# Optimization experiments

Hardware: AMD Instinct MI355X
Metric: run time of the kernel (lower is better)

The kernel has to match this reference:

```python
import jax, jax.numpy as jnp
import numpy as np

B, D, O = 8192, 64, 256

def setup_inputs() -> dict:
    key = jax.random.key(0)
    k1, k2, k3 = jax.random.split(key, 3)
    x = jax.random.normal(k1, (B, D), dtype=jnp.float32)
    centers = jax.random.uniform(k2, (O, 1, D), dtype=jnp.float32)  # RandomUniform(0,1)
    # Original uses Constant(10.0) which saturates exp(-quad) to 0; use small random
    # betas so the quadratic form is in a numerically meaningful range.
    betas = jax.random.normal(k3, (O, D, D), dtype=jnp.float32) * 0.05
    return {"x": x, "centers": centers, "betas": betas}

def reference(x, centers, betas):
    # precision[o] = betas[o] @ betas[o]^T   -> [O, D, D]
    precision = jnp.einsum('ode,ofe->odf', betas, betas)
    # diff[o,b,:] = centers[o] - x[b]        -> [O, B, D]
    diff = centers - x[None, :, :]
    # quad[o,b] = diff[o,b]^T P[o] diff[o,b] -> [O, B]
    quad = jnp.einsum('obd,odf,obf->ob', diff, precision, diff)
    return jnp.exp(-quad).T  # [B, O]
```

## Files before the change

kernel.cpp:

```cpp
#include <hip/hip_runtime.h>
#include <hip/hip_bf16.h>

typedef __bf16 bf16x8 __attribute__((ext_vector_type(8)));
typedef float  f32x4  __attribute__((ext_vector_type(4)));
typedef float  f32x16 __attribute__((ext_vector_type(16)));

constexpr int Bn = 8192, Dn = 64, On = 256;

#define GLD16(g, l) __builtin_amdgcn_global_load_lds( \
    (const __attribute__((address_space(1))) void*)(g), \
    (__attribute__((address_space(3))) void*)(l), 16, 0, 0)

__global__ void k_prep(const float* __restrict__ betas, const float* __restrict__ centers,
                       __bf16* __restrict__ bTsw, float* __restrict__ ncpk) {
    __shared__ float s[64 * 65];
    const int o = blockIdx.x, tid = threadIdx.x;
    const float* bo = betas + (size_t)o * 4096;
    for (int j = tid; j < 1024; j += 256) {
        int d = j >> 4, e4 = (j & 15) * 4;
        float4 v = ((const float4*)bo)[j];
        s[d * 65 + e4 + 0] = v.x; s[d * 65 + e4 + 1] = v.y;
        s[d * 65 + e4 + 2] = v.z; s[d * 65 + e4 + 3] = v.w;
    }
    __syncthreads();
    for (int p = tid; p < 4096; p += 256) {
        int chunk = p >> 3, j = p & 7;
        int ek = chunk >> 6, lane = chunk & 63;
        int e = (ek >> 2) * 32 + (lane & 31);
        int d = ((ek & 3) * 2 + (lane >> 5)) * 8 + j;
        bTsw[(size_t)o * 4096 + p] = (__bf16)s[d * 65 + e];
    }
    if (tid < 64) {
        int et = tid >> 5, rem = tid & 31, l5 = rem >> 4, reg = rem & 15;
        int row = et * 32 + l5 * 4 + (reg & 3) + ((reg >> 2) << 3);
        float acc = 0.f;
        for (int d = 0; d < 64; ++d) acc += s[d * 65 + row] * centers[o * 64 + d];
        ncpk[o * 64 + tid] = -acc;
    }
}

__global__ void __launch_bounds__(256, 4)
k_main(const float* __restrict__ x, const __bf16* __restrict__ bTsw,
       const float* __restrict__ ncpk, float* __restrict__ out) {
    __shared__ __align__(16) unsigned char smem[2 * 8192 + 2048];
    __bf16* sA0 = (__bf16*)smem;
    __bf16* sA1 = (__bf16*)(smem + 8192);
    float*  sCp = (float*)(smem + 16384);

    const int tid = threadIdx.x, wq = tid >> 6, lane = tid & 63;
    const int l31 = lane & 31, l5 = lane >> 5;
    const int bbase = blockIdx.x * 256;
    const int o0 = blockIdx.y * 8;

    sCp[tid]       = ncpk[o0 * 64 + tid];
    sCp[256 + tid] = ncpk[o0 * 64 + 256 + tid];

    bf16x8 xf[2][4];
#pragma unroll
    for (int bt = 0; bt < 2; ++bt)
#pragma unroll
        for (int kk = 0; kk < 4; ++kk) {
            const float* xp = x + (size_t)(bbase + wq * 64 + bt * 32 + l31) * 64
                                + (kk * 2 + l5) * 8;
            float4 v0 = *(const float4*)xp, v1 = *(const float4*)(xp + 4);
            bf16x8 f;
            f[0] = (__bf16)v0.x; f[1] = (__bf16)v0.y; f[2] = (__bf16)v0.z; f[3] = (__bf16)v0.w;
            f[4] = (__bf16)v1.x; f[5] = (__bf16)v1.y; f[6] = (__bf16)v1.z; f[7] = (__bf16)v1.w;
            xf[bt][kk] = f;
        }

    auto prefetch = [&](int o, __bf16* buf) {
        const __bf16* g = bTsw + (size_t)o * 4096;
        GLD16(g + (size_t)(wq * 128 + lane) * 8,      buf + (wq * 128) * 8);
        GLD16(g + (size_t)(wq * 128 + 64 + lane) * 8, buf + (wq * 128 + 64) * 8);
    };

    float qd[8];
    prefetch(o0, sA0);
    __builtin_amdgcn_s_waitcnt(0x0f70);
    __syncthreads();

#pragma unroll
    for (int oi = 0; oi < 8; ++oi) {
        __bf16* cur = (oi & 1) ? sA1 : sA0;
        if (oi < 7) prefetch(o0 + oi + 1, (oi & 1) ? sA0 : sA1);

        f32x4 qv[2] = {{0,0,0,0},{0,0,0,0}};
#pragma unroll
        for (int et = 0; et < 2; ++et) {
            f32x16 cpv;
#pragma unroll
            for (int r4 = 0; r4 < 4; ++r4)
                ((f32x4*)&cpv)[r4] = *(const f32x4*)(sCp + oi * 64 + et * 32 + l5 * 16 + r4 * 4);
            bf16x8 af[4];
#pragma unroll
            for (int k = 0; k < 4; ++k)
                af[k] = *(const bf16x8*)(cur + (size_t)((et * 4 + k) * 64 + lane) * 8);
#pragma unroll
            for (int bt = 0; bt < 2; ++bt) {
                f32x16 acc = __builtin_amdgcn_mfma_f32_32x32x16_bf16(af[0], xf[bt][0], cpv, 0, 0, 0);
                acc = __builtin_amdgcn_mfma_f32_32x32x16_bf16(af[1], xf[bt][1], acc, 0, 0, 0);
                acc = __builtin_amdgcn_mfma_f32_32x32x16_bf16(af[2], xf[bt][2], acc, 0, 0, 0);
                acc = __builtin_amdgcn_mfma_f32_32x32x16_bf16(af[3], xf[bt][3], acc, 0, 0, 0);
                const f32x4* aq = (const f32x4*)&acc;
                qv[bt] += aq[0] * aq[0];
                qv[bt] += aq[1] * aq[1];
                qv[bt] += aq[2] * aq[2];
                qv[bt] += aq[3] * aq[3];
            }
        }
        float q0 = (qv[0][0] + qv[0][1]) + (qv[0][2] + qv[0][3]);
        float q1 = (qv[1][0] + qv[1][1]) + (qv[1][2] + qv[1][3]);
        q0 += __shfl_xor(q0, 32, 64);
        q1 += __shfl_xor(q1, 32, 64);
        qd[oi] = l5 ? q1 : q0;

        __builtin_amdgcn_sched_barrier(0);
        __builtin_amdgcn_s_waitcnt(0x0f70);
        __syncthreads();
    }
    __syncthreads();

    float* scr = (float*)smem;
    {
        int r = wq * 64 + l5 * 32 + l31;
#pragma unroll
        for (int oi = 0; oi < 8; ++oi) scr[r * 12 + oi] = qd[oi];
    }
    __syncthreads();
    {
        const float* q8 = scr + tid * 12;
        f32x4 r0 = *(const f32x4*)q8, r1 = *(const f32x4*)(q8 + 4);
        f32x4 e0, e1;
#pragma unroll
        for (int j = 0; j < 4; ++j) { e0[j] = __expf(-r0[j]); e1[j] = __expf(-r1[j]); }
        float* op = out + (size_t)(bbase + tid) * 256 + o0;
        *(f32x4*)op       = e0;
        *(f32x4*)(op + 4) = e1;
    }
}

extern "C" void kernel_launch(void* const* d_in, const int* in_sizes, int n_in,
                              void* d_out, int out_size, void* d_ws, size_t ws_size,
                              hipStream_t stream) {
    const float* x       = (const float*)d_in[0];
    const float* centers = (const float*)d_in[1];
    const float* betas   = (const float*)d_in[2];
    float* out = (float*)d_out;

    char* ws = (char*)d_ws;
    __bf16* bTsw = (__bf16*)ws;
    float*  ncpk = (float*)(ws + 2 * (1 << 20));

    k_prep<<<dim3(On),                dim3(256), 0, stream>>>(betas, centers, bTsw, ncpk);
    k_main<<<dim3(Bn / 256, On / 8),  dim3(256), 0, stream>>>(x, bTsw, ncpk, out);
}
```

Measured before the change: 89.00 us.

## Expand quadratic form to drop per-output center loads and LDS epilogue

Rewrites the quadratic form as ||B^T x||^2 - 2 x·(B B^T c) + ||B^T c||^2. The main loop's MFMA accumulators therefore start from zero instead of per-output center projections loaded from LDS every iteration. The linear term is computed once per block with a few extra MFMAs, using hi/lo bf16-split weights prepared in k_prep. The constant term is precomputed in fp32. The redundant LDS round-trip in the epilogue is removed, and the affine term is combined via a lane shuffle. The risk is numerical cancellation from the expanded form, with x still quantized to bf16.

```diff
diff --git a/kernel.cpp b/kernel.cpp
--- a/kernel.cpp
+++ b/kernel.cpp
@@ -11,9 +11,15 @@
     (const __attribute__((address_space(1))) void*)(g), \
     (__attribute__((address_space(3))) void*)(l), 16, 0, 0)
 
+__device__ __forceinline__ int apos(int m, int d) {
+    return (((d >> 4) * 64) + (((d >> 3) & 1) * 32) + m) * 8 + (d & 7);
+}
+
 __global__ void k_prep(const float* __restrict__ betas, const float* __restrict__ centers,
-                       __bf16* __restrict__ bTsw, float* __restrict__ ncpk) {
+                       __bf16* __restrict__ bTsw, __bf16* __restrict__ waffT,
+                       float* __restrict__ kt) {
     __shared__ float s[64 * 65];
+    __shared__ float cp[64];
     const int o = blockIdx.x, tid = threadIdx.x;
     const float* bo = betas + (size_t)o * 4096;
     for (int j = tid; j < 1024; j += 256) {
@@ -21,6 +27,12 @@
         float4 v = ((const float4*)bo)[j];
         s[d * 65 + e4 + 0] = v.x; s[d * 65 + e4 + 1] = v.y;
         s[d * 65 + e4 + 2] = v.z; s[d * 65 + e4 + 3] = v.w;
+    }
+    __syncthreads();
+    if (tid < 64) {
+        float a = 0.f;
+        for (int d = 0; d < 64; ++d) a += s[d * 65 + tid] * centers[o * 64 + d];
+        cp[tid] = a;
     }
     __syncthreads();
     for (int p = tid; p < 4096; p += 256) {
@@ -31,29 +43,41 @@
         bTsw[(size_t)o * 4096 + p] = (__bf16)s[d * 65 + e];
     }
     if (tid < 64) {
-        int et = tid >> 5, rem = tid & 31, l5 = rem >> 4, reg = rem & 15;
-        int row = et * 32 + l5 * 4 + (reg & 3) + ((reg >> 2) << 3);
-        float acc = 0.f;
-        for (int d = 0; d < 64; ++d) acc += s[d * 65 + row] * centers[o * 64 + d];
-        ncpk[o * 64 + tid] = -acc;
+        int d = tid;
+        float w = 0.f;
+        for (int e = 0; e < 64; ++e) w += s[d * 65 + e] * cp[e];
+        w *= -2.f;
+        __bf16 hi = (__bf16)w;
+        __bf16 lo = (__bf16)(w - (float)hi);
+        size_t base = (size_t)(o >> 3) * 2048;
+        int m = o & 7;
+        waffT[base + apos(m, d)]      = hi;
+        waffT[base + apos(8 + m, d)]  = lo;
+        int mz = 16 + 2 * m;
+        waffT[base + apos(mz, d)]     = (__bf16)0.f;
+        waffT[base + apos(mz + 1, d)] = (__bf16)0.f;
+    }
+    if (tid == 0) {
+        float s2 = 0.f;
+        for (int e = 0; e < 64; ++e) s2 += cp[e] * cp[e];
+        kt[o] = s2;
     }
 }
 
 __global__ void __launch_bounds__(256, 4)
 k_main(const float* __restrict__ x, const __bf16* __restrict__ bTsw,
-       const float* __restrict__ ncpk, float* __restrict__ out) {
-    __shared__ __align__(16) unsigned char smem[2 * 8192 + 2048];
-    __bf16* sA0 = (__bf16*)smem;
-    __bf16* sA1 = (__bf16*)(smem + 8192);
-    float*  sCp = (float*)(smem + 16384);
+       const __bf16* __restrict__ waffT, const float* __restrict__ kt,
+       float* __restrict__ out) {
+    __shared__ __align__(16) __bf16 sA[2 * 4096];
+    __shared__ float sZero[4];
 
     const int tid = threadIdx.x, wq = tid >> 6, lane = tid & 63;
     const int l31 = lane & 31, l5 = lane >> 5;
     const int bbase = blockIdx.x * 256;
-    const int o0 = blockIdx.y * 8;
+    const int og = blockIdx.y;
+    const int o0 = og * 8;
 
-    sCp[tid]       = ncpk[o0 * 64 + tid];
-    sCp[256 + tid] = ncpk[o0 * 64 + 256 + tid];
+    if (tid < 4) sZero[tid] = 0.f;
 
     bf16x8 xf[2][4];
 #pragma unroll
@@ -68,6 +92,10 @@
             f[4] = (__bf16)v1.x; f[5] = (__bf16)v1.y; f[6] = (__bf16)v1.z; f[7] = (__bf16)v1.w;
             xf[bt][kk] = f;
         }
+    bf16x8 wf[4];
+#pragma unroll
+    for (int k = 0; k < 4; ++k)
+        wf[k] = *(const bf16x8*)(waffT + (size_t)og * 2048 + (size_t)(k * 64 + lane) * 8);
 
     auto prefetch = [&](int o, __bf16* buf) {
         const __bf16* g = bTsw + (size_t)o * 4096;
@@ -75,30 +103,43 @@
         GLD16(g + (size_t)(wq * 128 + 64 + lane) * 8, buf + (wq * 128 + 64) * 8);
     };
 
-    float qd[8];
-    prefetch(o0, sA0);
+    prefetch(o0, sA);
     __builtin_amdgcn_s_waitcnt(0x0f70);
     __syncthreads();
 
+    f32x4 z4 = *(const f32x4*)sZero;
+    f32x16 zc;
+#pragma unroll
+    for (int r4 = 0; r4 < 4; ++r4) ((f32x4*)&zc)[r4] = z4;
+
+    f32x4 aff4[2];
+#pragma unroll
+    for (int bt = 0; bt < 2; ++bt) {
+        f32x16 wa = __builtin_amdgcn_mfma_f32_32x32x16_bf16(wf[0], xf[bt][0], zc, 0, 0, 0);
+        wa = __builtin_amdgcn_mfma_f32_32x32x16_bf16(wf[1], xf[bt][1], wa, 0, 0, 0);
+        wa = __builtin_amdgcn_mfma_f32_32x32x16_bf16(wf[2], xf[bt][2], wa, 0, 0, 0);
+        wa = __builtin_amdgcn_mfma_f32_32x32x16_bf16(wf[3], xf[bt][3], wa, 0, 0, 0);
+#pragma unroll
+        for (int r = 0; r < 4; ++r)
+            aff4[bt][r] = wa[r] + wa[4 + r];
+    }
+
+    float qd[8];
 #pragma unroll
     for (int oi = 0; oi < 8; ++oi) {
-        __bf16* cur = (oi & 1) ? sA1 : sA0;
-        if (oi < 7) prefetch(o0 + oi + 1, (oi & 1) ? sA0 : sA1);
+        __bf16* cur = sA + (oi & 1) * 4096;
+        if (oi < 7) prefetch(o0 + oi + 1, sA + ((oi & 1) ^ 1) * 4096);
 
         f32x4 qv[2] = {{0,0,0,0},{0,0,0,0}};
 #pragma unroll
         for (int et = 0; et < 2; ++et) {
-            f32x16 cpv;
-#pragma unroll
-            for (int r4 = 0; r4 < 4; ++r4)
-                ((f32x4*)&cpv)[r4] = *(const f32x4*)(sCp + oi * 64 + et * 32 + l5 * 16 + r4 * 4);
             bf16x8 af[4];
 #pragma unroll
             for (int k = 0; k < 4; ++k)
                 af[k] = *(const bf16x8*)(cur + (size_t)((et * 4 + k) * 64 + lane) * 8);
 #pragma unroll
             for (int bt = 0; bt < 2; ++bt) {
-                f32x16 acc = __builtin_amdgcn_mfma_f32_32x32x16_bf16(af[0], xf[bt][0], cpv, 0, 0, 0);
+                f32x16 acc = __builtin_amdgcn_mfma_f32_32x32x16_bf16(af[0], xf[bt][0], zc, 0, 0, 0);
                 acc = __builtin_amdgcn_mfma_f32_32x32x16_bf16(af[1], xf[bt][1], acc, 0, 0, 0);
                 acc = __builtin_amdgcn_mfma_f32_32x32x16_bf16(af[2], xf[bt][2], acc, 0, 0, 0);
                 acc = __builtin_amdgcn_mfma_f32_32x32x16_bf16(af[3], xf[bt][3], acc, 0, 0, 0);
@@ -119,25 +160,24 @@
         __builtin_amdgcn_s_waitcnt(0x0f70);
         __syncthreads();
     }
-    __syncthreads();
 
-    float* scr = (float*)smem;
-    {
-        int r = wq * 64 + l5 * 32 + l31;
+    f32x4 affO = aff4[l5];
+    f32x4 affX;
 #pragma unroll
-        for (int oi = 0; oi < 8; ++oi) scr[r * 12 + oi] = qd[oi];
+    for (int r = 0; r < 4; ++r) affX[r] = __shfl_xor(aff4[l5 ^ 1][r], 32, 64);
+    f32x4 aff_lo = l5 ? affX : affO;
+    f32x4 aff_hi = l5 ? affO : affX;
+    f32x4 k_lo = *(const f32x4*)(kt + o0);
+    f32x4 k_hi = *(const f32x4*)(kt + o0 + 4);
+    f32x4 e0, e1;
+#pragma unroll
+    for (int j = 0; j < 4; ++j) {
+        e0[j] = __expf(-(qd[j]     + aff_lo[j] + k_lo[j]));
+        e1[j] = __expf(-(qd[4 + j] + aff_hi[j] + k_hi[j]));
     }
-    __syncthreads();
-    {
-        const float* q8 = scr + tid * 12;
-        f32x4 r0 = *(const f32x4*)q8, r1 = *(const f32x4*)(q8 + 4);
-        f32x4 e0, e1;
-#pragma unroll
-        for (int j = 0; j < 4; ++j) { e0[j] = __expf(-r0[j]); e1[j] = __expf(-r1[j]); }
-        float* op = out + (size_t)(bbase + tid) * 256 + o0;
-        *(f32x4*)op       = e0;
-        *(f32x4*)(op + 4) = e1;
-    }
+    float* op = out + (size_t)(bbase + tid) * 256 + o0;
+    *(f32x4*)op       = e0;
+    *(f32x4*)(op + 4) = e1;
 }
 
 extern "C" void kernel_launch(void* const* d_in, const int* in_sizes, int n_in,
@@ -149,9 +189,10 @@
     float* out = (float*)d_out;
 
     char* ws = (char*)d_ws;
-    __bf16* bTsw = (__bf16*)ws;
-    float*  ncpk = (float*)(ws + 2 * (1 << 20));
+    __bf16* bTsw  = (__bf16*)ws;
+    __bf16* waffT = (__bf16*)(ws + 2 * (1 << 20));
+    float*  ktab  = (float*)(ws + 2 * (1 << 20) + (128 << 10));
 
-    k_prep<<<dim3(On),                dim3(256), 0, stream>>>(betas, centers, bTsw, ncpk);
-    k_main<<<dim3(Bn / 256, On / 8),  dim3(256), 0, stream>>>(x, bTsw, ncpk, out);
+    k_prep<<<dim3(On),                dim3(256), 0, stream>>>(betas, centers, bTsw, waffT, ktab);
+    k_main<<<dim3(Bn / 256, On / 8),  dim3(256), 0, stream>>>(x, bTsw, waffT, ktab, out);
 }
```

Result: slower. 94.24 us (+5.9%).
